# Optimization experiments

Hardware: AMD Instinct MI355X
Metric: run time of the kernel (lower is better)

## Reference

```python
import jax, jax.numpy as jnp
import numpy as np

B, C, F, D = 128, 16, 128, 512


def setup_inputs() -> dict:
    key = jax.random.key(0)
    k1, k2 = jax.random.split(key)
    return {
        "c_feats": jax.random.normal(k1, (B, C, D), dtype=jnp.float32),
        "f_feats": jax.random.normal(k2, (B, F, D), dtype=jnp.float32),
    }


def _dtw_path_masks(S):
    """S: [P, c, f] per-pair similarity. Returns [P, c, f] 0/1 max-path masks.

    DP: D[i,j] = max(D[i-1,j], D[i,j-1], D[i-1,j-1]) + S[i-1,j-1], D[0,0]=0,
    borders -inf. Tie-break priority (up, left, diag) matches Python max().
    Row recurrence is vectorized: D[i,j] = Csum[j] + cummax_k<=j(A[k]-Csum[k-1])
    where A[k]=max(D[i-1,k], D[i-1,k-1]) (wavefront-free row-parallel form).
    """
    P_, c, f = S.shape
    NEG = -jnp.inf

    init = jnp.concatenate([jnp.zeros((P_, 1), S.dtype),
                            jnp.full((P_, f), NEG, S.dtype)], axis=1)  # D[0, 0..f]

    def row_step(prev, dt_row):
        # prev: [P, f+1] = D[i-1, 0..f]; dt_row: [P, f] = S[i-1, :]
        A = jnp.maximum(prev[:, 1:], prev[:, :-1])                  # max(D[i-1,j], D[i-1,j-1])
        Ccum = jnp.cumsum(dt_row, axis=1)
        Cm1 = jnp.concatenate([jnp.zeros((P_, 1), dt_row.dtype), Ccum[:, :-1]], axis=1)
        row = Ccum + jax.lax.cummax(A - Cm1, axis=1)                # D[i, 1..f]
        new_prev = jnp.concatenate([jnp.full((P_, 1), NEG, dt_row.dtype), row], axis=1)
        return new_prev, new_prev

    _, rows = jax.lax.scan(row_step, init, jnp.moveaxis(S, 1, 0))   # [c, P, f+1]
    Dm = jnp.moveaxis(jnp.concatenate([init[None], rows], axis=0), 1, 0)  # [P, c+1, f+1]

    # Predecessor choice per cell; argmax picks first max -> priority up,left,diag
    up = Dm[:, :-1, 1:]
    left = Dm[:, 1:, :-1]
    diag = Dm[:, :-1, :-1]
    mv = jnp.argmax(jnp.stack([up, left, diag], axis=-1), axis=-1).astype(jnp.int32)
    mv = jnp.pad(mv, ((0, 0), (1, 0), (1, 0)))                      # [P, c+1, f+1]

    pidx = jnp.arange(P_)

    def bt_step(carry, _):
        mask, i, j = carry
        active = (i > 0) | (j > 0)
        mask = mask.at[pidx, i - 1, j - 1].add(jnp.where(active, 1.0, 0.0).astype(mask.dtype))
        m = mv[pidx, i, j]
        di = jnp.where(m == 1, 0, 1)   # left keeps i
        dj = jnp.where(m == 0, 0, 1)   # up keeps j
        i = jnp.where(active, i - di, i)
        j = jnp.where(active, j - dj, j)
        return (mask, i, j), None

    mask0 = jnp.zeros((P_, c, f), jnp.float32)
    i0 = jnp.full((P_,), c, jnp.int32)
    j0 = jnp.full((P_,), f, jnp.int32)
    (mask, _, _), _ = jax.lax.scan(bt_step, (mask0, i0, j0), None, length=c + f)
    return mask


def reference(c_feats, f_feats):
    b, c, d = c_feats.shape
    f = f_feats.shape[1]
    xn = c_feats / jnp.linalg.norm(c_feats, axis=-1, keepdims=True)
    yn = f_feats / jnp.linalg.norm(f_feats, axis=-1, keepdims=True)
    # Source quirk: y row j is normalized only once outer index i reaches it
    # (y[i-1] bug), so S[i,j] uses normalized y[j] iff j <= i, raw y[j] otherwise.
    Sn = jnp.einsum('mcd,nfd->mncf', xn, yn)
    Sr = jnp.einsum('mcd,nfd->mncf', xn, f_feats)
    tri = jnp.arange(f)[None, :] <= jnp.arange(c)[:, None]          # [c, f]: j <= i
    S = jnp.where(tri, Sn, Sr).reshape(b * b, c, f)
    return _dtw_path_masks(S).reshape(b, b, c, f)
```

## Files before the change

kernel.cpp:

```cpp
#include <hip/hip_runtime.h>
#include <stdint.h>

#define M_TOT 2048
#define N_TOT 16384
#define K_TOT 512

typedef _Float16 f16x8 __attribute__((ext_vector_type(8)));
typedef float f32x4 __attribute__((ext_vector_type(4)));
typedef float f32x16 __attribute__((ext_vector_type(16)));

#define AS1 __attribute__((address_space(1)))
#define AS3 __attribute__((address_space(3)))

__device__ __forceinline__ void ld_lds16(const void* g, void* l) {
    __builtin_amdgcn_global_load_lds((const AS1 void*)g, (AS3 void*)l, 16, 0, 0);
}

__device__ __forceinline__ void split4(float x0, float x1, float x2, float x3,
                                       uint2* hs, uint2* ls) {
    union U { _Float16 h[4]; uint2 u; } H, L;
    _Float16 h0 = (_Float16)x0; H.h[0] = h0; L.h[0] = (_Float16)(x0 - (float)h0);
    _Float16 h1 = (_Float16)x1; H.h[1] = h1; L.h[1] = (_Float16)(x1 - (float)h1);
    _Float16 h2 = (_Float16)x2; H.h[2] = h2; L.h[2] = (_Float16)(x2 - (float)h2);
    _Float16 h3 = (_Float16)x3; H.h[3] = h3; L.h[3] = (_Float16)(x3 - (float)h3);
    *hs = H.u; *ls = L.u;
}

__global__ __launch_bounds__(256) void norm_split_kernel(
    const float* __restrict__ c_feats, const float* __restrict__ f_feats,
    _Float16* __restrict__ Ah, _Float16* __restrict__ Al,
    _Float16* __restrict__ Bh, _Float16* __restrict__ Bl,
    float* __restrict__ normf)
{
    int wave = blockIdx.x * 4 + (threadIdx.x >> 6);
    int lane = threadIdx.x & 63;
    if (wave < 2048) {
        const float* row = c_feats + (size_t)wave * K_TOT;
        float4 v0 = ((const float4*)row)[lane];
        float4 v1 = ((const float4*)row)[lane + 64];
        double ss = (double)v0.x * v0.x + (double)v0.y * v0.y +
                    (double)v0.z * v0.z + (double)v0.w * v0.w +
                    (double)v1.x * v1.x + (double)v1.y * v1.y +
                    (double)v1.z * v1.z + (double)v1.w * v1.w;
        #pragma unroll
        for (int off = 32; off; off >>= 1) ss += __shfl_down(ss, off);
        double tot = __shfl(ss, 0);
        float nrm = sqrtf((float)tot);
        float a0 = v0.x / nrm, a1 = v0.y / nrm, a2 = v0.z / nrm, a3 = v0.w / nrm;
        float b0 = v1.x / nrm, b1 = v1.y / nrm, b2 = v1.z / nrm, b3 = v1.w / nrm;
        uint2 h, l;
        split4(a0, a1, a2, a3, &h, &l);
        ((uint2*)(Ah + (size_t)wave * K_TOT))[lane] = h;
        ((uint2*)(Al + (size_t)wave * K_TOT))[lane] = l;
        split4(b0, b1, b2, b3, &h, &l);
        ((uint2*)(Ah + (size_t)wave * K_TOT))[lane + 64] = h;
        ((uint2*)(Al + (size_t)wave * K_TOT))[lane + 64] = l;
    } else if (wave < 18432) {
        int fr = wave - 2048;
        const float* row = f_feats + (size_t)fr * K_TOT;
        float4 v0 = ((const float4*)row)[lane];
        float4 v1 = ((const float4*)row)[lane + 64];
        double ss = (double)v0.x * v0.x + (double)v0.y * v0.y +
                    (double)v0.z * v0.z + (double)v0.w * v0.w +
                    (double)v1.x * v1.x + (double)v1.y * v1.y +
                    (double)v1.z * v1.z + (double)v1.w * v1.w;
        #pragma unroll
        for (int off = 32; off; off >>= 1) ss += __shfl_down(ss, off);
        if (lane == 0) normf[fr] = sqrtf((float)ss);
        uint2 h, l;
        split4(v0.x, v0.y, v0.z, v0.w, &h, &l);
        ((uint2*)(Bh + (size_t)fr * K_TOT))[lane] = h;
        ((uint2*)(Bl + (size_t)fr * K_TOT))[lane] = l;
        split4(v1.x, v1.y, v1.z, v1.w, &h, &l);
        ((uint2*)(Bh + (size_t)fr * K_TOT))[lane + 64] = h;
        ((uint2*)(Bl + (size_t)fr * K_TOT))[lane + 64] = l;
    }
}

__global__ __launch_bounds__(256, 4) void mfma_gemm_kernel(
    const _Float16* __restrict__ Ah, const _Float16* __restrict__ Al,
    const _Float16* __restrict__ Bh, const _Float16* __restrict__ Bl,
    const float* __restrict__ normf,
    float* __restrict__ out)
{
    __shared__ _Float16 sAh[128 * 32];
    __shared__ _Float16 sAl[128 * 32];
    __shared__ _Float16 sBh[128 * 32];
    __shared__ _Float16 sBl[128 * 32];

    const int t = threadIdx.x;
    const int w = t >> 6, lane = t & 63;
    const int ntile = ((blockIdx.x & 7) << 4) | (blockIdx.x >> 3);
    const int gm0 = blockIdx.y * 128, gn0 = ntile * 128;
    const int wm = (w & 1) * 64, wn = (w >> 1) * 64;
    const int m32 = lane & 31;
    const int kql0 = lane >> 5;

    f32x16 acc[2][2] = {};
    const int l0 = w * 128 + lane;

    for (int k0 = 0; k0 < K_TOT; k0 += 32) {
        #pragma unroll
        for (int c = 0; c < 2; ++c) {
            int l = l0 + c * 64;
            int lrow = l >> 2, kq = l & 3;
            int kqs = kq ^ ((lrow >> 1) & 3);
            size_t goffA = (size_t)(gm0 + lrow) * K_TOT + k0 + kqs * 8;
            size_t goffB = (size_t)(gn0 + lrow) * K_TOT + k0 + kqs * 8;
            ld_lds16(Ah + goffA, sAh + (size_t)l * 8);
            ld_lds16(Al + goffA, sAl + (size_t)l * 8);
            ld_lds16(Bh + goffB, sBh + (size_t)l * 8);
            ld_lds16(Bl + goffB, sBl + (size_t)l * 8);
        }
        __syncthreads();

        #pragma unroll
        for (int kh = 0; kh < 2; ++kh) {
            f16x8 fah[2], fal[2], fbh[2], fbl[2];
            #pragma unroll
            for (int x = 0; x < 2; ++x) {
                int arr = wm + x * 32 + m32;
                int brr = wn + x * 32 + m32;
                int kqa = (kh * 2 + kql0) ^ ((arr >> 1) & 3);
                int kqb = (kh * 2 + kql0) ^ ((brr >> 1) & 3);
                int ar = arr * 32 + kqa * 8;
                int br = brr * 32 + kqb * 8;
                fah[x] = *(const f16x8*)(sAh + ar);
                fal[x] = *(const f16x8*)(sAl + ar);
                fbh[x] = *(const f16x8*)(sBh + br);
                fbl[x] = *(const f16x8*)(sBl + br);
            }
            #pragma unroll
            for (int mi = 0; mi < 2; ++mi)
                #pragma unroll
                for (int ni = 0; ni < 2; ++ni) {
                    acc[mi][ni] = __builtin_amdgcn_mfma_f32_32x32x16_f16(fah[mi], fbl[ni], acc[mi][ni], 0, 0, 0);
                    acc[mi][ni] = __builtin_amdgcn_mfma_f32_32x32x16_f16(fal[mi], fbh[ni], acc[mi][ni], 0, 0, 0);
                    acc[mi][ni] = __builtin_amdgcn_mfma_f32_32x32x16_f16(fah[mi], fbh[ni], acc[mi][ni], 0, 0, 0);
                }
        }
        __syncthreads();
    }

    const int nn = ntile;
    const int rq = 4 * (lane >> 5);
    #pragma unroll
    for (int ni = 0; ni < 2; ++ni) {
        int col = wn + ni * 32 + m32;
        bool cn = (col < 16);
        float nf = cn ? normf[gn0 + col] : 1.f;
        #pragma unroll
        for (int mi = 0; mi < 2; ++mi) {
            #pragma unroll
            for (int reg = 0; reg < 16; ++reg) {
                int r = wm + mi * 32 + (reg & 3) + 8 * (reg >> 2) + rq;
                int gm = gm0 + r;
                int mm = gm >> 4, ii = gm & 15;
                float v = acc[mi][ni][reg];
                if (cn && col <= ii) v /= nf;
                out[(((size_t)mm * 128 + nn) * 16 + ii) * 128 + col] = v;
            }
        }
    }
}

#define WQS 296
#define WBUF 1184

__device__ __forceinline__ float dpp_shr1_f32(float x) {
    union { float f; int i; } u, v;
    u.f = x;
    v.i = __builtin_amdgcn_update_dpp(u.i, u.i, 0x111, 0xF, 0xF, false);
    return v.f;
}

__global__ __launch_bounds__(256) void dtw_kernel(float* __restrict__ buf)
{
    __shared__ float swin[4][2 * WBUF];
    __shared__ uint32_t mvw[4][4][132];
    __shared__ int bounds[4][4][16];

    const int lane = threadIdx.x & 63;
    const int w = threadIdx.x >> 6;
    const int q = lane >> 4, r = lane & 15;
    const int pbase = (1023 - blockIdx.x) * 16 + w * 4;
    const float4* gbase = (const float4*)(buf + (size_t)pbase * 2048);
    float* sw = swin[w];
    uint32_t* mvq = &mvw[w][q][0];

    int gidx[4], lidx[4];
    #pragma unroll
    for (int i = 0; i < 4; ++i) {
        gidx[i] = i * 512 + ((lane >> 2) & 15) * 32 + (lane & 3);
        lidx[i] = i * WQS + ((lane >> 2) & 15) * 18 + (lane & 3) * 4;
    }

#define WSTORE(regs, boff)                                                      \
    {                                                                           \
        _Pragma("unroll")                                                       \
        for (int i = 0; i < 4; ++i) {                                           \
            *(float2*)(sw + (boff) + lidx[i])     = make_float2(regs[i].x, regs[i].y); \
            *(float2*)(sw + (boff) + lidx[i] + 2) = make_float2(regs[i].z, regs[i].w); \
        }                                                                       \
    }
#define WLOAD(regs, win)                                                        \
    {                                                                           \
        _Pragma("unroll")                                                       \
        for (int i = 0; i < 4; ++i) regs[i] = gbase[gidx[i] + (win) * 4];       \
    }

    float4 ga[4], gb[4];
    WLOAD(ga, 0)
    WLOAD(gb, 1)
    WSTORE(ga, 0)
    WSTORE(gb, WBUF)
    WLOAD(ga, 2)
    WLOAD(gb, 3)

    const float NEG = -1e30f;
    float Dp = NEG, rawprev = NEG;
    uint32_t mvbuf = 0;
    int j = -r;
    const int sb = q * WQS + r * 18;

#define DTW_STEP(BOUNDARY)                                                      \
    {                                                                           \
        float upr = dpp_shr1_f32(Dp);                                           \
        float dg = rawprev;                                                     \
        rawprev = upr;                                                          \
        float up = (r == 0) ? NEG : upr;                                        \
        float lf = Dp;                                                          \
        if (BOUNDARY) {                                                         \
            if (j == 0) { lf = NEG; dg = (r == 0) ? 0.0f : NEG; }               \
            else if (r == 0) dg = NEG;                                          \
        } else {                                                                \
            if (r == 0) dg = NEG;                                               \
        }                                                                       \
        float sv = sw[(((j >> 4) & 1) ? WBUF : 0) + sb + (j & 15)];             \
        int m = (up >= lf && up >= dg) ? 0 : ((lf >= dg) ? 1 : 2);              \
        float Dc = fmaxf(up, fmaxf(lf, dg)) + sv;                               \
        if ((unsigned)j < 128u) {                                               \
            mvbuf |= (uint32_t)m << (2 * (j & 15));                             \
            if ((j & 15) == 15) { mvq[r * 8 + (j >> 4)] = mvbuf; mvbuf = 0; }   \
        }                                                                       \
        Dp = Dc;                                                                \
        ++j;                                                                    \
    }

    for (int t = 0; t < 16; ++t) DTW_STEP(true)
    for (int t = 16; t < 32; ++t) DTW_STEP(false)
    WSTORE(ga, 0)        WLOAD(ga, 4)
    for (int t = 32; t < 48; ++t) DTW_STEP(false)
    WSTORE(gb, WBUF)     WLOAD(gb, 5)
    for (int t = 48; t < 64; ++t) DTW_STEP(false)
    WSTORE(ga, 0)        WLOAD(ga, 6)
    for (int t = 64; t < 80; ++t) DTW_STEP(false)
    WSTORE(gb, WBUF)     WLOAD(gb, 7)
    for (int t = 80; t < 96; ++t) DTW_STEP(false)
    WSTORE(ga, 0)
    for (int t = 96; t < 112; ++t) DTW_STEP(false)
    WSTORE(gb, WBUF)
    for (int t = 112; t < 143; ++t) DTW_STEP(false)
#undef DTW_STEP
#undef WSTORE
#undef WLOAD

    __syncthreads();

    if (r == 0) {
        int i = 16, jj = 128, hic = 127;
        int cidx = -1;
        uint32_t word = 0;
        for (int it = 0; it < 160; ++it) {
            if (i <= 0) break;
            int idx = (i - 1) * 8 + ((jj - 1) >> 4);
            if (idx != cidx) { word = mvq[idx]; cidx = idx; }
            int m = (int)((word >> (2 * ((jj - 1) & 15))) & 3u);
            if (m == 1) { --jj; continue; }
            bounds[w][q][i - 1] = (jj - 1) | (hic << 8);
            if (m == 2) --jj;
            --i;
            hic = jj - 1;
        }
    }
    __syncthreads();

    #pragma unroll 4
    for (int it = 0; it < 32; ++it) {
        int flat = it * 64 + lane;
        int q2 = flat >> 9;
        int rem = flat & 511;
        int ii = rem >> 5;
        int c4 = rem & 31;
        int b = bounds[w][q2][ii];
        int lo = b & 0xff, hi = (b >> 8) & 0xff;
        int j0 = c4 * 4;
        float4 v;
        v.x = (j0 + 0 >= lo && j0 + 0 <= hi) ? 1.f : 0.f;
        v.y = (j0 + 1 >= lo && j0 + 1 <= hi) ? 1.f : 0.f;
        v.z = (j0 + 2 >= lo && j0 + 2 <= hi) ? 1.f : 0.f;
        v.w = (j0 + 3 >= lo && j0 + 3 <= hi) ? 1.f : 0.f;
        float* tb = buf + (size_t)(pbase + q2) * 2048;
        *(float4*)(tb + ii * 128 + j0) = v;
    }
}

extern "C" void kernel_launch(void* const* d_in, const int* in_sizes, int n_in,
                              void* d_out, int out_size, void* d_ws, size_t ws_size,
                              hipStream_t stream)
{
    const float* c_feats = (const float*)d_in[0];
    const float* f_feats = (const float*)d_in[1];
    float* out = (float*)d_out;

    _Float16* Ah = (_Float16*)d_ws;
    _Float16* Al = Ah + (size_t)M_TOT * K_TOT;
    _Float16* Bh = Al + (size_t)M_TOT * K_TOT;
    _Float16* Bl = Bh + (size_t)N_TOT * K_TOT;
    float* normf = (float*)(Bl + (size_t)N_TOT * K_TOT);

    norm_split_kernel<<<4608, 256, 0, stream>>>(c_feats, f_feats, Ah, Al, Bh, Bl, normf);
    dim3 g(N_TOT / 128, M_TOT / 128);
    mfma_gemm_kernel<<<g, 256, 0, stream>>>(Ah, Al, Bh, Bl, normf, out);
    dtw_kernel<<<1024, 256, 0, stream>>>(out);
}
```

Baseline: 339.1 us.

## Rewrite split-fp16 GEMM with 256x256 tiles and 4-stage LDS pipeline

The GEMM kernel now uses 512-thread blocks computing 256x256 output tiles with K-step 16. It keeps a 4-deep ring of LDS buffers filled via global_load_lds, with explicit vmcnt waits, split barriers and setprio around MFMA groups so loads overlap compute. The goal is to hide global load latency and raise MFMA utilisation compared with the synchronous 128x128 loop. The change also retunes the DTW window constants (WQS/WBUF). Risks: more barriers per K step, higher register and LDS pressure lowering occupancy, and fragile hand-counted waitcnts.

```diff
diff --git a/kernel.cpp b/kernel.cpp
--- a/kernel.cpp
+++ b/kernel.cpp
@@ -14,6 +14,12 @@
 
 __device__ __forceinline__ void ld_lds16(const void* g, void* l) {
     __builtin_amdgcn_global_load_lds((const AS1 void*)g, (AS3 void*)l, 16, 0, 0);
+}
+
+__device__ __forceinline__ void wg_barrier() {
+    asm volatile("" ::: "memory");
+    __builtin_amdgcn_s_barrier();
+    asm volatile("" ::: "memory");
 }
 
 __device__ __forceinline__ void split4(float x0, float x1, float x2, float x3,
@@ -77,85 +83,141 @@
     }
 }
 
-__global__ __launch_bounds__(256, 4) void mfma_gemm_kernel(
+__global__ __launch_bounds__(512, 2) void mfma_gemm_kernel(
     const _Float16* __restrict__ Ah, const _Float16* __restrict__ Al,
     const _Float16* __restrict__ Bh, const _Float16* __restrict__ Bl,
     const float* __restrict__ normf,
     float* __restrict__ out)
 {
-    __shared__ _Float16 sAh[128 * 32];
-    __shared__ _Float16 sAl[128 * 32];
-    __shared__ _Float16 sBh[128 * 32];
-    __shared__ _Float16 sBl[128 * 32];
+    __shared__ _Float16 sA[4 * 2 * 4096];
+    __shared__ _Float16 sB[4 * 2 * 4096];
 
     const int t = threadIdx.x;
     const int w = t >> 6, lane = t & 63;
-    const int ntile = ((blockIdx.x & 7) << 4) | (blockIdx.x >> 3);
-    const int gm0 = blockIdx.y * 128, gn0 = ntile * 128;
-    const int wm = (w & 1) * 64, wn = (w >> 1) * 64;
-    const int m32 = lane & 31;
-    const int kql0 = lane >> 5;
-
-    f32x16 acc[2][2] = {};
-    const int l0 = w * 128 + lane;
-
-    for (int k0 = 0; k0 < K_TOT; k0 += 32) {
+    const int m32 = lane & 31, kql0 = lane >> 5;
+    const int rq = 4 * kql0;
+
+    const int bid = (int)blockIdx.x;
+    const int swz = (bid & 7) * 64 + (bid >> 3);
+    const int gm0 = (swz >> 6) * 256;
+    const int gn0 = (swz & 63) * 256;
+    const int wm = (w & 1) * 128, wn = (w >> 1) * 64;
+
+    const int slrow = t >> 1, skq = t & 1;
+    const int skqs = skq ^ ((slrow >> 2) & 1);
+    const _Float16* gAh = Ah + (size_t)(gm0 + slrow) * K_TOT + skqs * 8;
+    const _Float16* gAl = Al + (size_t)(gm0 + slrow) * K_TOT + skqs * 8;
+    const _Float16* gBh = Bh + (size_t)(gn0 + slrow) * K_TOT + skqs * 8;
+    const _Float16* gBl = Bl + (size_t)(gn0 + slrow) * K_TOT + skqs * 8;
+    _Float16* const dA = sA + t * 8;
+    _Float16* const dB = sB + t * 8;
+
+    int offA[4], offB[2];
+    #pragma unroll
+    for (int mi = 0; mi < 4; ++mi) {
+        int rr = wm + mi * 32 + m32;
+        offA[mi] = rr * 16 + (kql0 ^ ((rr >> 2) & 1)) * 8;
+    }
+    #pragma unroll
+    for (int ni = 0; ni < 2; ++ni) {
+        int rr = wn + ni * 32 + m32;
+        offB[ni] = rr * 16 + (kql0 ^ ((rr >> 2) & 1)) * 8;
+    }
+
+    f32x16 acc[4][2] = {};
+
+    #pragma unroll
+    for (int pt = 0; pt < 3; ++pt) {
+        ld_lds16(gAh + pt * 16, dA + pt * 8192);
+        ld_lds16(gAl + pt * 16, dA + pt * 8192 + 4096);
+        ld_lds16(gBh + pt * 16, dB + pt * 8192);
+        ld_lds16(gBl + pt * 16, dB + pt * 8192 + 4096);
+    }
+    asm volatile("s_waitcnt vmcnt(8)" ::: "memory");
+    __builtin_amdgcn_s_barrier();
+    asm volatile("" ::: "memory");
+
+#define MFMA_QUAD(MH)                                                           \
+    _Pragma("unroll")                                                           \
+    for (int mi2 = 0; mi2 < 2; ++mi2) {                                         \
+        _Pragma("unroll")                                                       \
+        for (int ni = 0; ni < 2; ++ni) {                                        \
+            acc[(MH)*2 + mi2][ni] = __builtin_amdgcn_mfma_f32_32x32x16_f16(     \
+                fa[mi2][0], fB0[ni][1], acc[(MH)*2 + mi2][ni], 0, 0, 0);        \
+            acc[(MH)*2 + mi2][ni] = __builtin_amdgcn_mfma_f32_32x32x16_f16(     \
+                fa[mi2][1], fB0[ni][0], acc[(MH)*2 + mi2][ni], 0, 0, 0);        \
+            acc[(MH)*2 + mi2][ni] = __builtin_amdgcn_mfma_f32_32x32x16_f16(     \
+                fa[mi2][0], fB0[ni][0], acc[(MH)*2 + mi2][ni], 0, 0, 0);        \
+        }                                                                       \
+    }
+
+#define TILE_BODY(KT, DO_STAGE, VMASM)                                          \
+    {                                                                           \
+        const int buf_ = (KT) & 3;                                              \
+        const _Float16* lA = sA + buf_ * 8192;                                  \
+        const _Float16* lB = sB + buf_ * 8192;                                  \
+        f16x8 fB0[2][2], fa[2][2];                                              \
+        _Pragma("unroll")                                                       \
+        for (int ni = 0; ni < 2; ++ni) {                                        \
+            fB0[ni][0] = *(const f16x8*)(lB + offB[ni]);                        \
+            fB0[ni][1] = *(const f16x8*)(lB + 4096 + offB[ni]);                 \
+        }                                                                       \
+        _Pragma("unroll")                                                       \
+        for (int mi2 = 0; mi2 < 2; ++mi2) {                                     \
+            fa[mi2][0] = *(const f16x8*)(lA + offA[mi2]);                       \
+            fa[mi2][1] = *(const f16x8*)(lA + 4096 + offA[mi2]);                \
+        }                                                                       \
+        if (DO_STAGE) {                                                         \
+            const int nb_ = ((KT) + 3) & 3;                                     \
+            ld_lds16(gAh + ((KT) + 3) * 16, dA + nb_ * 8192);                   \
+            ld_lds16(gAl + ((KT) + 3) * 16, dA + nb_ * 8192 + 4096);            \
+        }                                                                       \
+        wg_barrier();                                                           \
+        __builtin_amdgcn_s_setprio(1);                                          \
+        MFMA_QUAD(0)                                                            \
+        __builtin_amdgcn_s_setprio(0);                                          \
+        wg_barrier();                                                           \
+        _Pragma("unroll")                                                       \
+        for (int mi2 = 0; mi2 < 2; ++mi2) {                                     \
+            fa[mi2][0] = *(const f16x8*)(lA + offA[2 + mi2]);                   \
+            fa[mi2][1] = *(const f16x8*)(lA + 4096 + offA[2 + mi2]);            \
+        }                                                                       \
+        if (DO_STAGE) {                                                         \
+            const int nb_ = ((KT) + 3) & 3;                                     \
+            ld_lds16(gBh + ((KT) + 3) * 16, dB + nb_ * 8192);                   \
+            ld_lds16(gBl + ((KT) + 3) * 16, dB + nb_ * 8192 + 4096);            \
+        }                                                                       \
+        wg_barrier();                                                           \
+        __builtin_amdgcn_s_setprio(1);                                          \
+        MFMA_QUAD(1)                                                            \
+        __builtin_amdgcn_s_setprio(0);                                          \
+        asm volatile(VMASM ::: "memory");                                       \
+        wg_barrier();                                                           \
+    }
+
+    #pragma unroll 1
+    for (int kt = 0; kt < 29; ++kt)
+        TILE_BODY(kt, 1, "s_waitcnt vmcnt(8)")
+    TILE_BODY(29, 0, "s_waitcnt vmcnt(4)")
+    TILE_BODY(30, 0, "s_waitcnt vmcnt(0)")
+    TILE_BODY(31, 0, "")
+
+#undef TILE_BODY
+#undef MFMA_QUAD
+
+    #pragma unroll
+    for (int ni = 0; ni < 2; ++ni) {
+        const int gc = gn0 + wn + ni * 32 + m32;
+        const int col = gc & 127;
+        const int nn = gc >> 7;
+        const bool cn = (col < 16);
+        const float nf = cn ? normf[gc] : 1.f;
         #pragma unroll
-        for (int c = 0; c < 2; ++c) {
-            int l = l0 + c * 64;
-            int lrow = l >> 2, kq = l & 3;
-            int kqs = kq ^ ((lrow >> 1) & 3);
-            size_t goffA = (size_t)(gm0 + lrow) * K_TOT + k0 + kqs * 8;
-            size_t goffB = (size_t)(gn0 + lrow) * K_TOT + k0 + kqs * 8;
-            ld_lds16(Ah + goffA, sAh + (size_t)l * 8);
-            ld_lds16(Al + goffA, sAl + (size_t)l * 8);
-            ld_lds16(Bh + goffB, sBh + (size_t)l * 8);
-            ld_lds16(Bl + goffB, sBl + (size_t)l * 8);
-        }
-        __syncthreads();
-
-        #pragma unroll
-        for (int kh = 0; kh < 2; ++kh) {
-            f16x8 fah[2], fal[2], fbh[2], fbl[2];
-            #pragma unroll
-            for (int x = 0; x < 2; ++x) {
-                int arr = wm + x * 32 + m32;
-                int brr = wn + x * 32 + m32;
-                int kqa = (kh * 2 + kql0) ^ ((arr >> 1) & 3);
-                int kqb = (kh * 2 + kql0) ^ ((brr >> 1) & 3);
-                int ar = arr * 32 + kqa * 8;
-                int br = brr * 32 + kqb * 8;
-                fah[x] = *(const f16x8*)(sAh + ar);
-                fal[x] = *(const f16x8*)(sAl + ar);
-                fbh[x] = *(const f16x8*)(sBh + br);
-                fbl[x] = *(const f16x8*)(sBl + br);
-            }
-            #pragma unroll
-            for (int mi = 0; mi < 2; ++mi)
-                #pragma unroll
-                for (int ni = 0; ni < 2; ++ni) {
-                    acc[mi][ni] = __builtin_amdgcn_mfma_f32_32x32x16_f16(fah[mi], fbl[ni], acc[mi][ni], 0, 0, 0);
-                    acc[mi][ni] = __builtin_amdgcn_mfma_f32_32x32x16_f16(fal[mi], fbh[ni], acc[mi][ni], 0, 0, 0);
-                    acc[mi][ni] = __builtin_amdgcn_mfma_f32_32x32x16_f16(fah[mi], fbh[ni], acc[mi][ni], 0, 0, 0);
-                }
-        }
-        __syncthreads();
-    }
-
-    const int nn = ntile;
-    const int rq = 4 * (lane >> 5);
-    #pragma unroll
-    for (int ni = 0; ni < 2; ++ni) {
-        int col = wn + ni * 32 + m32;
-        bool cn = (col < 16);
-        float nf = cn ? normf[gn0 + col] : 1.f;
-        #pragma unroll
-        for (int mi = 0; mi < 2; ++mi) {
+        for (int mi = 0; mi < 4; ++mi) {
             #pragma unroll
             for (int reg = 0; reg < 16; ++reg) {
-                int r = wm + mi * 32 + (reg & 3) + 8 * (reg >> 2) + rq;
-                int gm = gm0 + r;
-                int mm = gm >> 4, ii = gm & 15;
+                const int gm = gm0 + wm + mi * 32 + (reg & 3) + 8 * (reg >> 2) + rq;
+                const int mm = gm >> 4, ii = gm & 15;
                 float v = acc[mi][ni][reg];
                 if (cn && col <= ii) v /= nf;
                 out[(((size_t)mm * 128 + nn) * 16 + ii) * 128 + col] = v;
@@ -164,8 +226,8 @@
     }
 }
 
-#define WQS 296
-#define WBUF 1184
+#define WQS 304
+#define WBUF 1216
 
 __device__ __forceinline__ float dpp_shr1_f32(float x) {
     union { float f; int i; } u, v;
@@ -320,7 +382,6 @@
     float* normf = (float*)(Bl + (size_t)N_TOT * K_TOT);
 
     norm_split_kernel<<<4608, 256, 0, stream>>>(c_feats, f_feats, Ah, Al, Bh, Bl, normf);
-    dim3 g(N_TOT / 128, M_TOT / 128);
-    mfma_gemm_kernel<<<g, 256, 0, stream>>>(Ah, Al, Bh, Bl, normf, out);
+    mfma_gemm_kernel<<<512, 512, 0, stream>>>(Ah, Al, Bh, Bl, normf, out);
     dtw_kernel<<<1024, 256, 0, stream>>>(out);
 }
```

Result: slower. 349.4 us (+3.0%).
